# Kernel tuning notes

Hardware: AMD Instinct MI355X
Metric: run time of the kernel (lower is better)

The kernel has to match this reference:

```python
import jax, jax.numpy as jnp
import numpy as np

N, E, D, G, L, ED = 20000, 640000, 128, 128, 5, 7
BN_EPS = 1e-5


def _bn(x, g, b):
    # training-mode BatchNorm1d: biased batch statistics
    m = x.mean(axis=0)
    v = jnp.mean((x - m) ** 2, axis=0)
    return g * (x - m) / jnp.sqrt(v + BN_EPS) + b


def setup_inputs() -> dict:
    key = jax.random.key(0)
    ks = jax.random.split(key, 16)
    s = 0.05
    p = {}
    p["x"] = jax.random.normal(ks[0], (N, D), jnp.float32)
    p["edge_attr"] = jax.random.normal(ks[1], (E, ED), jnp.float32)
    p["edge_index"] = jax.random.randint(ks[2], (2, E), 0, N, jnp.int32)
    p["batch"] = jnp.sort(jax.random.randint(ks[3], (N,), 0, G, jnp.int32))
    p["enc_W"] = jax.random.normal(ks[4], (D, D), jnp.float32) * s
    p["enc_b"] = jnp.zeros((D,), jnp.float32)
    p["vn_emb"] = jnp.zeros((1, D), jnp.float32)  # init.constant_(0)
    p["eps"] = jnp.zeros((L,), jnp.float32)       # GIN eps init 0
    p["edge_W"] = jax.random.normal(ks[5], (L, ED, D), jnp.float32) * s
    p["edge_b"] = jnp.zeros((L, D), jnp.float32)
    p["mlp_W1"] = jax.random.normal(ks[6], (L, D, 2 * D), jnp.float32) * s
    p["mlp_b1"] = jnp.zeros((L, 2 * D), jnp.float32)
    p["mlp_bn1_g"] = jnp.ones((L, 2 * D), jnp.float32)
    p["mlp_bn1_b"] = jnp.zeros((L, 2 * D), jnp.float32)
    p["mlp_W2"] = jax.random.normal(ks[7], (L, 2 * D, D), jnp.float32) * s
    p["mlp_b2"] = jnp.zeros((L, D), jnp.float32)
    p["bn_g"] = jnp.ones((L, D), jnp.float32)
    p["bn_b"] = jnp.zeros((L, D), jnp.float32)
    p["vn_W1"] = jax.random.normal(ks[8], (L - 1, D, 2 * D), jnp.float32) * s
    p["vn_b1"] = jnp.zeros((L - 1, 2 * D), jnp.float32)
    p["vn_bn1_g"] = jnp.ones((L - 1, 2 * D), jnp.float32)
    p["vn_bn1_b"] = jnp.zeros((L - 1, 2 * D), jnp.float32)
    p["vn_W2"] = jax.random.normal(ks[9], (L - 1, 2 * D, D), jnp.float32) * s
    p["vn_b2"] = jnp.zeros((L - 1, D), jnp.float32)
    p["vn_bn2_g"] = jnp.ones((L - 1, D), jnp.float32)
    p["vn_bn2_b"] = jnp.zeros((L - 1, D), jnp.float32)
    return p


def reference(x, edge_attr, edge_index, batch, enc_W, enc_b, vn_emb, eps,
              edge_W, edge_b, mlp_W1, mlp_b1, mlp_bn1_g, mlp_bn1_b, mlp_W2,
              mlp_b2, bn_g, bn_b, vn_W1, vn_b1, vn_bn1_g, vn_bn1_b, vn_W2,
              vn_b2, vn_bn2_g, vn_bn2_b):
    src, dst = edge_index[0], edge_index[1]
    h = x @ enc_W + enc_b                       # node_encoder (Linear)
    vn = jnp.broadcast_to(vn_emb[0], (G, D))    # virtual node per graph, init 0
    for l in range(L):
        h_in = h + vn[batch]                    # gather virtual node into nodes
        # GINConv: message = relu(x_j + edge_emb), aggr='add'
        eemb = edge_attr @ edge_W[l] + edge_b[l]            # [E, D]
        msg = jax.nn.relu(h_in[src] + eemb)                 # [E, D]
        agg = jax.ops.segment_sum(msg, dst, num_segments=N) # scatter-add
        z = (1.0 + eps[l]) * h_in + agg
        z = jax.nn.relu(_bn(z @ mlp_W1[l] + mlp_b1[l], mlp_bn1_g[l], mlp_bn1_b[l]))
        z = z @ mlp_W2[l] + mlp_b2[l]
        hn = _bn(z, bn_g[l], bn_b[l])           # outer BatchNorm1d
        if l < L - 1:
            hn = jax.nn.relu(hn)                # relu on all but last layer
            # virtual node update: global_add_pool over h_list[layer] (= h_in)
            pooled = jax.ops.segment_sum(h_in, batch, num_segments=G) + vn
            t = jax.nn.relu(_bn(pooled @ vn_W1[l] + vn_b1[l], vn_bn1_g[l], vn_bn1_b[l]))
            vn = jax.nn.relu(_bn(t @ vn_W2[l] + vn_b2[l], vn_bn2_g[l], vn_bn2_b[l]))
        h = hn
    return h  # JK='last' node representation [N, D]
```

## Files before the change

### kernel.cpp

```cpp
#include <hip/hip_runtime.h>

#define N_NODES 20000
#define N_EDGES 640000
#define DIM 128
#define NGRAPH 128
#define NLAYER 5
#define EDIM 7
#define TWO_D 256

typedef __bf16 bf16x8 __attribute__((ext_vector_type(8)));
typedef __bf16 bf16x4 __attribute__((ext_vector_type(4)));
typedef __bf16 bf16x2 __attribute__((ext_vector_type(2)));
typedef float  f32x4  __attribute__((ext_vector_type(4)));

__device__ __forceinline__ f32x4 mfma16(bf16x8 a, bf16x8 b, f32x4 c) {
  return __builtin_amdgcn_mfma_f32_16x16x32_bf16(a, b, c, 0, 0, 0);
}

__global__ void k_hist(const int* __restrict__ dst, int* __restrict__ counts) {
  int e = blockIdx.x * blockDim.x + threadIdx.x;
  if (e < N_EDGES) atomicAdd(&counts[dst[e]], 1);
}

__global__ __launch_bounds__(1024) void k_scanA(const int* __restrict__ counts,
    int* __restrict__ local, int* __restrict__ bsum) {
  __shared__ int sd[1024];
  int b = blockIdx.x, tid = threadIdx.x;
  int i = b * 1024 + tid;
  int v = (i < N_NODES) ? counts[i] : 0;
  sd[tid] = v;
  __syncthreads();
  for (int ofs = 1; ofs < 1024; ofs <<= 1) {
    int t = (tid >= ofs) ? sd[tid - ofs] : 0;
    __syncthreads();
    sd[tid] += t;
    __syncthreads();
  }
  if (i <= N_NODES) local[i] = sd[tid] - v;
  if (tid == 1023) bsum[b] = sd[1023];
}

__global__ void k_scanB(int* __restrict__ bsum, int* __restrict__ carry,
                        int* __restrict__ offsets) {
  if (threadIdx.x == 0) {
    int run = 0;
    for (int b = 0; b < 20; ++b) { carry[b] = run; run += bsum[b]; }
    offsets[N_NODES] = run;
  }
}

__global__ __launch_bounds__(1024) void k_scanC(const int* __restrict__ local,
    const int* __restrict__ carry, int* __restrict__ offsets) {
  int i = blockIdx.x * 1024 + threadIdx.x;
  if (i < N_NODES) offsets[i] = local[i] + carry[i >> 10];
}

__global__ void k_fillA(const int* __restrict__ dstArr, const int* __restrict__ offsets,
                        int* __restrict__ cursor, int* __restrict__ perm) {
  int e = blockIdx.x * blockDim.x + threadIdx.x;
  if (e >= N_EDGES) return;
  int d = dstArr[e];
  int p = offsets[d] + atomicAdd(&cursor[d], 1);
  perm[p] = e;
}

__global__ void k_fillB(const int* __restrict__ perm, const int* __restrict__ srcArr,
                        const float* __restrict__ edge_attr,
                        int* __restrict__ csr_src, __bf16* __restrict__ ea_csr) {
  int i = blockIdx.x * blockDim.x + threadIdx.x;
  if (i >= N_EDGES) return;
  int e = perm[i];
  csr_src[i] = srcArr[e];
  const float* ea = edge_attr + (size_t)e * EDIM;
  bf16x8 v;
#pragma unroll
  for (int k = 0; k < EDIM; ++k) v[k] = (__bf16)ea[k];
  v[7] = (__bf16)0.f;
  *(bf16x8*)(ea_csr + (size_t)i * 8) = v;
}

__global__ void k_gs(const int* __restrict__ batch, int* __restrict__ gs) {
  int g = threadIdx.x;
  if (g > NGRAPH) return;
  if (g == NGRAPH) { gs[NGRAPH] = N_NODES; return; }
  int lo = 0, hi = N_NODES;
  while (lo < hi) { int mid = (lo + hi) >> 1; if (batch[mid] < g) lo = mid + 1; else hi = mid; }
  gs[g] = lo;
}

__global__ void k_convT2(const float* __restrict__ src, __bf16* __restrict__ dst_hi,
                         __bf16* __restrict__ dst_lo, int K, int C, int layers) {
  int total = layers * K * C;
  for (int i = blockIdx.x * blockDim.x + threadIdx.x; i < total;
       i += gridDim.x * blockDim.x) {
    int l = i / (K * C);
    int rem = i - l * K * C;
    int k = rem / C;
    int c = rem - k * C;
    float v = src[i];
    __bf16 hi = (__bf16)v;
    __bf16 lo = (__bf16)(v - (float)hi);
    size_t o = (size_t)l * K * C + (size_t)c * K + k;
    dst_hi[o] = hi;
    dst_lo[o] = lo;
  }
}

__global__ void k_vninit(const float* __restrict__ vn_emb, float* __restrict__ vn) {
  int i = blockIdx.x * blockDim.x + threadIdx.x;
  if (i < NGRAPH * DIM) vn[i] = vn_emb[i & (DIM - 1)];
}

__global__ __launch_bounds__(128) void k_enc(const float* __restrict__ x,
    const __bf16* __restrict__ encT_hi, const __bf16* __restrict__ encT_lo,
    const float* __restrict__ enc_b, const float* __restrict__ vn_emb,
    float* __restrict__ h_in, __bf16* __restrict__ h_bf) {
  int lane = threadIdx.x & 63, wid = threadIdx.x >> 6;
  int rbase = blockIdx.x * 32 + wid * 16;
  int r = rbase + (lane & 15);
  int ko = (lane >> 4) * 8;
  const float* xr = x + (size_t)r * DIM;
  bf16x8 a_hi[4], a_lo[4];
#pragma unroll
  for (int ks = 0; ks < 4; ++ks) {
    f32x4 v0 = *(const f32x4*)(xr + ks * 32 + ko);
    f32x4 v1 = *(const f32x4*)(xr + ks * 32 + ko + 4);
    bf16x8 th, tl;
#pragma unroll
    for (int j = 0; j < 4; ++j) {
      th[j] = (__bf16)v0[j];     tl[j] = (__bf16)(v0[j] - (float)th[j]);
      th[4+j] = (__bf16)v1[j];   tl[4+j] = (__bf16)(v1[j] - (float)th[4+j]);
    }
    a_hi[ks] = th; a_lo[ks] = tl;
  }
  const f32x4 fz = {0.f, 0.f, 0.f, 0.f};
  f32x4 acc[8];
#pragma unroll
  for (int nf = 0; nf < 8; ++nf) acc[nf] = fz;
#pragma unroll
  for (int nf = 0; nf < 8; ++nf) {
    size_t wrow = (size_t)(nf * 16 + (lane & 15)) * DIM + ko;
    const __bf16* bh = encT_hi + wrow;
    const __bf16* bl = encT_lo + wrow;
#pragma unroll
    for (int ks = 0; ks < 4; ++ks) {
      bf16x8 wh = *(const bf16x8*)(bh + ks * 32);
      bf16x8 wl = *(const bf16x8*)(bl + ks * 32);
      acc[nf] = mfma16(a_hi[ks], wh, acc[nf]);
      acc[nf] = mfma16(a_lo[ks], wh, acc[nf]);
      acc[nf] = mfma16(a_hi[ks], wl, acc[nf]);
    }
  }
  int c0 = lane & 15;
  int rr = rbase + (lane >> 4) * 4;
#pragma unroll
  for (int nf = 0; nf < 8; ++nf) {
    int c = nf * 16 + c0;
    float bias = enc_b[c] + vn_emb[c];
#pragma unroll
    for (int j = 0; j < 4; ++j) {
      float v = acc[nf][j] + bias;
      h_in[(size_t)(rr + j) * DIM + c] = v;
      h_bf[(size_t)(rr + j) * DIM + c] = (__bf16)v;
    }
  }
}

__global__ __launch_bounds__(1024) void k_pool(const __bf16* __restrict__ h_bf,
    const int* __restrict__ gs, const float* __restrict__ vnbuf,
    const float* __restrict__ vnr, const float* __restrict__ sv2,
    const float* __restrict__ qv2, const float* __restrict__ bn2g,
    const float* __restrict__ bn2b, int use_stats,
    float* __restrict__ pooled) {
  __shared__ float red[8][DIM];
  __shared__ float vns[DIM];
  int tid = threadIdx.x;
  int g = blockIdx.x;
  if (tid < DIM) {
    if (use_stats) {
      float s = 0.f, q = 0.f;
#pragma unroll
      for (int rep = 0; rep < 8; ++rep) { s += sv2[rep * DIM + tid]; q += qv2[rep * DIM + tid]; }
      float m = s * (1.f / NGRAPH);
      float var = q * (1.f / NGRAPH) - m * m;
      float a = bn2g[tid] / sqrtf(var + 1e-5f);
      vns[tid] = fmaxf(vnr[g * DIM + tid] * a + (bn2b[tid] - m * a), 0.f);
    } else {
      vns[tid] = vnbuf[g * DIM + tid];
    }
  }
  __syncthreads();
  int d = tid & 127, slot = tid >> 7;
  int lo = gs[g], hi = gs[g + 1];
  float acc = 0.f;
  for (int n = lo + slot; n < hi; n += 8)
    acc += (float)h_bf[(size_t)n * DIM + d];
  red[slot][d] = acc;
  __syncthreads();
  if (slot == 0) {
    float t = vns[d];
#pragma unroll
    for (int s2 = 0; s2 < 8; ++s2) t += red[s2][d];
    pooled[g * DIM + d] = t;
  }
}

__global__ __launch_bounds__(256) void k_agg(const __bf16* __restrict__ h_bf,
    const float* __restrict__ h_in, const int* __restrict__ offsets,
    const int* __restrict__ csr_src, const __bf16* __restrict__ ea_csr,
    const float* __restrict__ eW, const float* __restrict__ eB,
    const float* __restrict__ eps, int l,
    __bf16* __restrict__ z_hi, __bf16* __restrict__ z_lo) {
  int tid = threadIdx.x;
  int lane = tid & 63, w = tid >> 6;
  int l2 = lane * 2;
  int n = blockIdx.x * 4 + w;
  float w0[EDIM], w1[EDIM];
#pragma unroll
  for (int k = 0; k < EDIM; ++k) {
    float2 wv = *(const float2*)(eW + k * DIM + l2);
    w0[k] = wv.x; w1[k] = wv.y;
  }
  float2 ebv = *(const float2*)(eB + l2);
  int off = offsets[n], end = offsets[n + 1];
  float acc0 = 0.f, acc1 = 0.f;

  auto edge = [&](int iu) {
    int s = csr_src[iu];
    const unsigned* eu = (const unsigned*)(ea_csr + (size_t)iu * 8);
    unsigned u0 = eu[0], u1 = eu[1], u2 = eu[2], u3 = eu[3];
    unsigned hv = *(const unsigned*)(h_bf + (size_t)s * DIM + l2);
    float e0 = __builtin_bit_cast(float, u0 << 16);
    float e1 = __builtin_bit_cast(float, u0 & 0xffff0000u);
    float e2 = __builtin_bit_cast(float, u1 << 16);
    float e3 = __builtin_bit_cast(float, u1 & 0xffff0000u);
    float e4 = __builtin_bit_cast(float, u2 << 16);
    float e5 = __builtin_bit_cast(float, u2 & 0xffff0000u);
    float e6 = __builtin_bit_cast(float, u3 << 16);
    float m0 = __builtin_bit_cast(float, hv << 16) + ebv.x;
    float m1 = __builtin_bit_cast(float, hv & 0xffff0000u) + ebv.y;
    m0 = fmaf(e0, w0[0], m0); m1 = fmaf(e0, w1[0], m1);
    m0 = fmaf(e1, w0[1], m0); m1 = fmaf(e1, w1[1], m1);
    m0 = fmaf(e2, w0[2], m0); m1 = fmaf(e2, w1[2], m1);
    m0 = fmaf(e3, w0[3], m0); m1 = fmaf(e3, w1[3], m1);
    m0 = fmaf(e4, w0[4], m0); m1 = fmaf(e4, w1[4], m1);
    m0 = fmaf(e5, w0[5], m0); m1 = fmaf(e5, w1[5], m1);
    m0 = fmaf(e6, w0[6], m0); m1 = fmaf(e6, w1[6], m1);
    acc0 += fmaxf(m0, 0.f);
    acc1 += fmaxf(m1, 0.f);
  };

  int i = off;
  for (; i + 7 < end; i += 8) {
    int iu = __builtin_amdgcn_readfirstlane(i);
    edge(iu);     edge(iu + 1); edge(iu + 2); edge(iu + 3);
    edge(iu + 4); edge(iu + 5); edge(iu + 6); edge(iu + 7);
  }
  for (; i < end; ++i) {
    edge(__builtin_amdgcn_readfirstlane(i));
  }
  float epsv = 1.f + eps[l];
  float2 hs = *(const float2*)(h_in + (size_t)n * DIM + l2);
  float v0 = epsv * hs.x + acc0;
  float v1 = epsv * hs.y + acc1;
  __bf16 hi0 = (__bf16)v0, hi1 = (__bf16)v1;
  bf16x2 zh; zh[0] = hi0; zh[1] = hi1;
  bf16x2 zl; zl[0] = (__bf16)(v0 - (float)hi0); zl[1] = (__bf16)(v1 - (float)hi1);
  *(bf16x2*)(z_hi + (size_t)n * DIM + l2) = zh;
  *(bf16x2*)(z_lo + (size_t)n * DIM + l2) = zl;
}

__global__ __launch_bounds__(256) void k_gemm1(const __bf16* __restrict__ z_hi,
    const __bf16* __restrict__ z_lo,
    const __bf16* __restrict__ W1T_hi, const __bf16* __restrict__ W1T_lo,
    const float* __restrict__ b1,
    float* __restrict__ y1, float* __restrict__ s1, float* __restrict__ q1) {
  int tid = threadIdx.x;
  int lane = tid & 63, wid = tid >> 6;
  int rowH = wid >> 1, colH = wid & 1;
  int rbase = blockIdx.x * 32 + rowH * 16;
  int r = rbase + (lane & 15);
  int ko = (lane >> 4) * 8;
  bf16x8 a_hi[4], a_lo[4];
#pragma unroll
  for (int ks = 0; ks < 4; ++ks) {
    a_hi[ks] = *(const bf16x8*)(z_hi + (size_t)r * DIM + ks * 32 + ko);
    a_lo[ks] = *(const bf16x8*)(z_lo + (size_t)r * DIM + ks * 32 + ko);
  }
  const f32x4 fz = {0.f, 0.f, 0.f, 0.f};
  f32x4 acc[8];
#pragma unroll
  for (int nf8 = 0; nf8 < 8; ++nf8) acc[nf8] = fz;
#pragma unroll
  for (int nf8 = 0; nf8 < 8; ++nf8) {
    int nf = colH * 8 + nf8;
    size_t wrow = (size_t)(nf * 16 + (lane & 15)) * DIM + ko;
    const __bf16* bh = W1T_hi + wrow;
    const __bf16* bl = W1T_lo + wrow;
#pragma unroll
    for (int ks = 0; ks < 4; ++ks) {
      bf16x8 wh = *(const bf16x8*)(bh + ks * 32);
      bf16x8 wl = *(const bf16x8*)(bl + ks * 32);
      acc[nf8] = mfma16(a_hi[ks], wh, acc[nf8]);
      acc[nf8] = mfma16(a_lo[ks], wh, acc[nf8]);
      acc[nf8] = mfma16(a_hi[ks], wl, acc[nf8]);
    }
  }
  int c0 = lane & 15;
  int rr = rbase + (lane >> 4) * 4;
  int rep = blockIdx.x & 7;
#pragma unroll
  for (int nf8 = 0; nf8 < 8; ++nf8) {
    int c = (colH * 8 + nf8) * 16 + c0;
    float bias = b1[c];
    float s = 0.f, q = 0.f;
#pragma unroll
    for (int j = 0; j < 4; ++j) {
      float v = acc[nf8][j] + bias;
      y1[(size_t)(rr + j) * TWO_D + c] = v;
      s += v; q += v * v;
    }
    s += __shfl_xor(s, 16); s += __shfl_xor(s, 32);
    q += __shfl_xor(q, 16); q += __shfl_xor(q, 32);
    if (lane < 16) {
      atomicAdd(&s1[rep * TWO_D + c], s);
      atomicAdd(&q1[rep * TWO_D + c], q);
    }
  }
}

__global__ __launch_bounds__(256) void k_gemm2(const float* __restrict__ y1,
    const __bf16* __restrict__ W2T_hi, const __bf16* __restrict__ W2T_lo,
    const float* __restrict__ b2,
    const float* __restrict__ s1, const float* __restrict__ q1,
    const float* __restrict__ bn1g, const float* __restrict__ bn1b,
    float* __restrict__ y2, float* __restrict__ s2, float* __restrict__ q2) {
  __shared__ float sc1s[TWO_D], sh1s[TWO_D];
  int tid = threadIdx.x;
  {
    int c = tid;
    float s = 0.f, q = 0.f;
#pragma unroll
    for (int rep = 0; rep < 8; ++rep) { s += s1[rep * TWO_D + c]; q += q1[rep * TWO_D + c]; }
    float m = s * (1.f / N_NODES);
    float var = q * (1.f / N_NODES) - m * m;
    float a = bn1g[c] / sqrtf(var + 1e-5f);
    sc1s[c] = a; sh1s[c] = bn1b[c] - m * a;
  }
  __syncthreads();
  int lane = tid & 63, wid = tid >> 6;
  int rowH = wid >> 1, colH = wid & 1;
  int rbase = blockIdx.x * 32 + rowH * 16;
  int r = rbase + (lane & 15);
  int ko = (lane >> 4) * 8;
  bf16x8 a_hi[8], a_lo[8];
#pragma unroll
  for (int ks = 0; ks < 8; ++ks) {
    int kb = ks * 32 + ko;
    f32x4 r0 = *(const f32x4*)(y1 + (size_t)r * TWO_D + kb);
    f32x4 r1 = *(const f32x4*)(y1 + (size_t)r * TWO_D + kb + 4);
    f32x4 sc0 = *(const f32x4*)(&sc1s[kb]);
    f32x4 sc1 = *(const f32x4*)(&sc1s[kb + 4]);
    f32x4 sh0 = *(const f32x4*)(&sh1s[kb]);
    f32x4 sh1 = *(const f32x4*)(&sh1s[kb + 4]);
    bf16x8 th, tl;
#pragma unroll
    for (int j = 0; j < 4; ++j) {
      float v0 = fmaxf(r0[j] * sc0[j] + sh0[j], 0.f);
      float v1 = fmaxf(r1[j] * sc1[j] + sh1[j], 0.f);
      th[j] = (__bf16)v0;     tl[j] = (__bf16)(v0 - (float)th[j]);
      th[4+j] = (__bf16)v1;   tl[4+j] = (__bf16)(v1 - (float)th[4+j]);
    }
    a_hi[ks] = th; a_lo[ks] = tl;
  }
  const f32x4 fz = {0.f, 0.f, 0.f, 0.f};
  f32x4 acc[4];
#pragma unroll
  for (int nf4 = 0; nf4 < 4; ++nf4) acc[nf4] = fz;
#pragma unroll
  for (int nf4 = 0; nf4 < 4; ++nf4) {
    int nf = colH * 4 + nf4;
    size_t wrow = (size_t)(nf * 16 + (lane & 15)) * TWO_D + ko;
    const __bf16* bh = W2T_hi + wrow;
    const __bf16* bl = W2T_lo + wrow;
#pragma unroll
    for (int ks = 0; ks < 8; ++ks) {
      bf16x8 wh = *(const bf16x8*)(bh + ks * 32);
      bf16x8 wl = *(const bf16x8*)(bl + ks * 32);
      acc[nf4] = mfma16(a_hi[ks], wh, acc[nf4]);
      acc[nf4] = mfma16(a_lo[ks], wh, acc[nf4]);
      acc[nf4] = mfma16(a_hi[ks], wl, acc[nf4]);
    }
  }
  int c0 = lane & 15;
  int rr = rbase + (lane >> 4) * 4;
  int rep = blockIdx.x & 7;
#pragma unroll
  for (int nf4 = 0; nf4 < 4; ++nf4) {
    int c = (colH * 4 + nf4) * 16 + c0;
    float bias = b2[c];
    float s = 0.f, q = 0.f;
#pragma unroll
    for (int j = 0; j < 4; ++j) {
      float v = acc[nf4][j] + bias;
      y2[(size_t)(rr + j) * DIM + c] = v;
      s += v; q += v * v;
    }
    s += __shfl_xor(s, 16); s += __shfl_xor(s, 32);
    q += __shfl_xor(q, 16); q += __shfl_xor(q, 32);
    if (lane < 16) {
      atomicAdd(&s2[rep * DIM + c], s);
      atomicAdd(&q2[rep * DIM + c], q);
    }
  }
}

__global__ __launch_bounds__(256) void k_vgemm1(const float* __restrict__ pooled,
    const float* __restrict__ W1, const float* __restrict__ b1,
    float* __restrict__ tv, float* __restrict__ sv1, float* __restrict__ qv1) {
  __shared__ float row[DIM];
  int g = blockIdx.x, tid = threadIdx.x;
  if (tid < DIM) row[tid] = pooled[g * DIM + tid];
  __syncthreads();
  int c = tid;
  float acc = b1[c];
  for (int k = 0; k < DIM; ++k) acc = fmaf(row[k], W1[k * TWO_D + c], acc);
  tv[g * TWO_D + c] = acc;
  int rep = g & 7;
  atomicAdd(&sv1[rep * TWO_D + c], acc);
  atomicAdd(&qv1[rep * TWO_D + c], acc * acc);
}

__global__ __launch_bounds__(256) void k_vgemm2(const float* __restrict__ tv,
    const float* __restrict__ sv1, const float* __restrict__ qv1,
    const float* __restrict__ bn1g, const float* __restrict__ bn1b,
    const float* __restrict__ W2, const float* __restrict__ b2,
    float* __restrict__ vnr, float* __restrict__ sv2, float* __restrict__ qv2) {
  __shared__ float trow[TWO_D];
  int g = blockIdx.x, tid = threadIdx.x;
  {
    float s = 0.f, q = 0.f;
#pragma unroll
    for (int rep = 0; rep < 8; ++rep) { s += sv1[rep * TWO_D + tid]; q += qv1[rep * TWO_D + tid]; }
    float m = s * (1.f / NGRAPH);
    float var = q * (1.f / NGRAPH) - m * m;
    float a = bn1g[tid] / sqrtf(var + 1e-5f);
    trow[tid] = fmaxf(tv[g * TWO_D + tid] * a + (bn1b[tid] - m * a), 0.f);
  }
  __syncthreads();
  if (tid < DIM) {
    float acc = b2[tid];
    for (int k = 0; k < TWO_D; ++k) acc = fmaf(trow[k], W2[k * DIM + tid], acc);
    vnr[g * DIM + tid] = acc;
    int rep = g & 7;
    atomicAdd(&sv2[rep * DIM + tid], acc);
    atomicAdd(&qv2[rep * DIM + tid], acc * acc);
  }
}

__global__ __launch_bounds__(256) void k_bn2hin(const float* __restrict__ y2,
    const float* __restrict__ s2, const float* __restrict__ q2,
    const float* __restrict__ bng, const float* __restrict__ bnb,
    const float* __restrict__ vnr, const float* __restrict__ sv2,
    const float* __restrict__ qv2, const float* __restrict__ vbn2g,
    const float* __restrict__ vbn2b, const int* __restrict__ batch,
    float* __restrict__ h_in, __bf16* __restrict__ h_bf) {
  __shared__ float sc2s[DIM], sh2s[DIM], scvn[DIM], shvn[DIM];
  int tid = threadIdx.x;
  if (tid < DIM) {
    float s = 0.f, q = 0.f;
#pragma unroll
    for (int rep = 0; rep < 8; ++rep) { s += s2[rep * DIM + tid]; q += q2[rep * DIM + tid]; }
    float m = s * (1.f / N_NODES);
    float var = q * (1.f / N_NODES) - m * m;
    float a = bng[tid] / sqrtf(var + 1e-5f);
    sc2s[tid] = a; sh2s[tid] = bnb[tid] - m * a;
    float sv = 0.f, qv = 0.f;
#pragma unroll
    for (int rep = 0; rep < 8; ++rep) { sv += sv2[rep * DIM + tid]; qv += qv2[rep * DIM + tid]; }
    float mv = sv * (1.f / NGRAPH);
    float varv = qv * (1.f / NGRAPH) - mv * mv;
    float av = vbn2g[tid] / sqrtf(varv + 1e-5f);
    scvn[tid] = av; shvn[tid] = vbn2b[tid] - mv * av;
  }
  __syncthreads();
  int idx = blockIdx.x * 256 + tid;
  if (idx >= N_NODES * (DIM / 4)) return;
  int c4 = idx & 31;
  int row = idx >> 5;
  f32x4 y = ((const f32x4*)y2)[idx];
  f32x4 scv = ((const f32x4*)sc2s)[c4];
  f32x4 shv = ((const f32x4*)sh2s)[c4];
  f32x4 vsc = ((const f32x4*)scvn)[c4];
  f32x4 vsh = ((const f32x4*)shvn)[c4];
  int b = batch[row];
  f32x4 vr = ((const f32x4*)vnr)[b * 32 + c4];
  f32x4 o;
  bf16x4 ob;
#pragma unroll
  for (int j = 0; j < 4; ++j) {
    float vnv = fmaxf(vr[j] * vsc[j] + vsh[j], 0.f);
    o[j] = fmaxf(y[j] * scv[j] + shv[j], 0.f) + vnv;
    ob[j] = (__bf16)o[j];
  }
  ((f32x4*)h_in)[idx] = o;
  ((bf16x4*)h_bf)[idx] = ob;
}

__global__ __launch_bounds__(256) void k_out(const float* __restrict__ y2,
    const float* __restrict__ s2, const float* __restrict__ q2,
    const float* __restrict__ bng, const float* __restrict__ bnb,
    float* __restrict__ out) {
  __shared__ float sc2s[DIM], sh2s[DIM];
  int tid = threadIdx.x;
  if (tid < DIM) {
    float s = 0.f, q = 0.f;
#pragma unroll
    for (int rep = 0; rep < 8; ++rep) { s += s2[rep * DIM + tid]; q += q2[rep * DIM + tid]; }
    float m = s * (1.f / N_NODES);
    float var = q * (1.f / N_NODES) - m * m;
    float a = bng[tid] / sqrtf(var + 1e-5f);
    sc2s[tid] = a; sh2s[tid] = bnb[tid] - m * a;
  }
  __syncthreads();
  int idx = blockIdx.x * 256 + tid;
  if (idx >= N_NODES * (DIM / 4)) return;
  int c4 = idx & 31;
  f32x4 y = ((const f32x4*)y2)[idx];
  f32x4 scv = ((const f32x4*)sc2s)[c4];
  f32x4 shv = ((const f32x4*)sh2s)[c4];
  f32x4 o;
#pragma unroll
  for (int j = 0; j < 4; ++j) o[j] = y[j] * scv[j] + shv[j];
  ((f32x4*)out)[idx] = o;
}

extern "C" void kernel_launch(void* const* d_in, const int* in_sizes, int n_in,
                              void* d_out, int out_size, void* d_ws, size_t ws_size,
                              hipStream_t stream) {
  const float* x         = (const float*)d_in[0];
  const float* edge_attr = (const float*)d_in[1];
  const int*   edge_index= (const int*)d_in[2];
  const int*   batch     = (const int*)d_in[3];
  const float* enc_W     = (const float*)d_in[4];
  const float* enc_b     = (const float*)d_in[5];
  const float* vn_emb    = (const float*)d_in[6];
  const float* eps       = (const float*)d_in[7];
  const float* edge_W    = (const float*)d_in[8];
  const float* edge_b    = (const float*)d_in[9];
  const float* mlp_W1    = (const float*)d_in[10];
  const float* mlp_b1    = (const float*)d_in[11];
  const float* mlp_bn1_g = (const float*)d_in[12];
  const float* mlp_bn1_b = (const float*)d_in[13];
  const float* mlp_W2    = (const float*)d_in[14];
  const float* mlp_b2    = (const float*)d_in[15];
  const float* bn_g      = (const float*)d_in[16];
  const float* bn_b      = (const float*)d_in[17];
  const float* vn_W1     = (const float*)d_in[18];
  const float* vn_b1     = (const float*)d_in[19];
  const float* vn_bn1_g  = (const float*)d_in[20];
  const float* vn_bn1_b  = (const float*)d_in[21];
  const float* vn_W2     = (const float*)d_in[22];
  const float* vn_b2     = (const float*)d_in[23];
  const float* vn_bn2_g  = (const float*)d_in[24];
  const float* vn_bn2_b  = (const float*)d_in[25];

  char* wsb = (char*)d_ws;
  size_t off = 0;
  auto take = [&](size_t bytes) -> void* {
    void* p = wsb + off;
    off += (bytes + 255) & ~(size_t)255;
    return p;
  };
  float*  h_in    = (float*)take((size_t)N_NODES * DIM * 4);
  float*  y2      = (float*)take((size_t)N_NODES * DIM * 4);
  float*  y1      = (float*)take((size_t)N_NODES * TWO_D * 4);
  __bf16* h_bf    = (__bf16*)y1;
  __bf16* z_hi    = (__bf16*)take((size_t)N_NODES * DIM * 2);
  __bf16* z_lo    = (__bf16*)take((size_t)N_NODES * DIM * 2);
  int*    csr_src = (int*)take((size_t)N_EDGES * 4);
  __bf16* ea_csr  = (__bf16*)take((size_t)N_EDGES * 8 * 2);
  int*    perm    = (int*)take((size_t)N_EDGES * 4);
  int*    counts  = (int*)take((size_t)2 * N_NODES * 4);
  int*    cursor  = counts + N_NODES;
  int*    offsets = (int*)take((size_t)(N_NODES + 1) * 4);
  int*    slocal  = (int*)take((size_t)(N_NODES + 1024) * 4);
  int*    sbsum   = (int*)take(64 * 4);
  int*    scarry  = sbsum + 32;
  int*    gs      = (int*)take((size_t)(NGRAPH + 1) * 4);
  float*  pooled  = (float*)take((size_t)NGRAPH * DIM * 4);
  float*  tv      = (float*)take((size_t)NGRAPH * TWO_D * 4);
  float*  vnr     = (float*)take((size_t)NGRAPH * DIM * 4);
  float*  vn0     = (float*)take((size_t)NGRAPH * DIM * 4);
  float*  stats   = (float*)take((size_t)NLAYER * 12288 * 4);
  __bf16* encT_hi = (__bf16*)take((size_t)DIM * DIM * 2);
  __bf16* encT_lo = (__bf16*)take((size_t)DIM * DIM * 2);
  __bf16* W1T_hi  = (__bf16*)take((size_t)NLAYER * DIM * TWO_D * 2);
  __bf16* W1T_lo  = (__bf16*)take((size_t)NLAYER * DIM * TWO_D * 2);
  __bf16* W2T_hi  = (__bf16*)take((size_t)NLAYER * TWO_D * DIM * 2);
  __bf16* W2T_lo  = (__bf16*)take((size_t)NLAYER * TWO_D * DIM * 2);
  if (off > ws_size) return;

  const int* srcArr = edge_index;
  const int* dstArr = edge_index + N_EDGES;

  hipMemsetAsync(counts, 0, (size_t)2 * N_NODES * 4, stream);
  hipMemsetAsync(stats, 0, (size_t)NLAYER * 12288 * 4, stream);

  k_hist<<<N_EDGES / 256, 256, 0, stream>>>(dstArr, counts);
  k_scanA<<<20, 1024, 0, stream>>>(counts, slocal, sbsum);
  k_scanB<<<1, 64, 0, stream>>>(sbsum, scarry, offsets);
  k_scanC<<<20, 1024, 0, stream>>>(slocal, scarry, offsets);
  k_fillA<<<N_EDGES / 256, 256, 0, stream>>>(dstArr, offsets, cursor, perm);
  k_fillB<<<N_EDGES / 256, 256, 0, stream>>>(perm, srcArr, edge_attr, csr_src, ea_csr);
  k_gs<<<1, 256, 0, stream>>>(batch, gs);
  k_convT2<<<128, 256, 0, stream>>>(enc_W, encT_hi, encT_lo, DIM, DIM, 1);
  k_convT2<<<128, 256, 0, stream>>>(mlp_W1, W1T_hi, W1T_lo, DIM, TWO_D, NLAYER);
  k_convT2<<<128, 256, 0, stream>>>(mlp_W2, W2T_hi, W2T_lo, TWO_D, DIM, NLAYER);
  k_vninit<<<(NGRAPH * DIM) / 256, 256, 0, stream>>>(vn_emb, vn0);
  k_enc<<<N_NODES / 32, 128, 0, stream>>>(x, encT_hi, encT_lo, enc_b, vn_emb, h_in, h_bf);

  for (int l = 0; l < NLAYER; ++l) {
    float* s1  = stats + (size_t)l * 12288;
    float* q1  = s1 + 2048;
    float* s2  = s1 + 4096;
    float* q2  = s1 + 5120;
    float* sv1 = s1 + 6144;
    float* qv1 = s1 + 8192;
    float* sv2 = s1 + 10240;
    float* qv2 = s1 + 11264;
    if (l < NLAYER - 1) {
      if (l == 0)
        k_pool<<<NGRAPH, 1024, 0, stream>>>(h_bf, gs, vn0, vn0, nullptr, nullptr,
            nullptr, nullptr, 0, pooled);
      else {
        float* psv2 = stats + (size_t)(l - 1) * 12288 + 10240;
        float* pqv2 = stats + (size_t)(l - 1) * 12288 + 11264;
        k_pool<<<NGRAPH, 1024, 0, stream>>>(h_bf, gs, vn0, vnr, psv2, pqv2,
            vn_bn2_g + (size_t)(l - 1) * DIM, vn_bn2_b + (size_t)(l - 1) * DIM, 1, pooled);
      }
    }
    k_agg<<<N_NODES / 4, 256, 0, stream>>>(h_bf, h_in, offsets, csr_src, ea_csr,
        edge_W + (size_t)l * EDIM * DIM, edge_b + (size_t)l * DIM, eps, l, z_hi, z_lo);
    k_gemm1<<<N_NODES / 32, 256, 0, stream>>>(z_hi, z_lo,
        W1T_hi + (size_t)l * DIM * TWO_D, W1T_lo + (size_t)l * DIM * TWO_D,
        mlp_b1 + (size_t)l * TWO_D, y1, s1, q1);
    k_gemm2<<<N_NODES / 32, 256, 0, stream>>>(y1,
        W2T_hi + (size_t)l * TWO_D * DIM, W2T_lo + (size_t)l * TWO_D * DIM,
        mlp_b2 + (size_t)l * DIM, s1, q1,
        mlp_bn1_g + (size_t)l * TWO_D, mlp_bn1_b + (size_t)l * TWO_D,
        y2, s2, q2);
    if (l < NLAYER - 1) {
      k_vgemm1<<<NGRAPH, 256, 0, stream>>>(pooled, vn_W1 + (size_t)l * DIM * TWO_D,
          vn_b1 + (size_t)l * TWO_D, tv, sv1, qv1);
      k_vgemm2<<<NGRAPH, 256, 0, stream>>>(tv, sv1, qv1,
          vn_bn1_g + (size_t)l * TWO_D, vn_bn1_b + (size_t)l * TWO_D,
          vn_W2 + (size_t)l * TWO_D * DIM, vn_b2 + (size_t)l * DIM,
          vnr, sv2, qv2);
      k_bn2hin<<<(N_NODES * 32) / 256, 256, 0, stream>>>(y2, s2, q2,
          bn_g + (size_t)l * DIM, bn_b + (size_t)l * DIM,
          vnr, sv2, qv2, vn_bn2_g + (size_t)l * DIM, vn_bn2_b + (size_t)l * DIM,
          batch, h_in, h_bf);
    } else {
      k_out<<<(N_NODES * 32) / 256, 256, 0, stream>>>(y2, s2, q2,
          bn_g + (size_t)l * DIM, bn_b + (size_t)l * DIM, (float*)d_out);
    }
  }
}
```

Before: 738.9 us.

## Store activations as bf16 hi/lo pairs and merge setup kernels

Result: no change. 740.5 us (+0.2%).

```diff
diff --git a/kernel.cpp b/kernel.cpp
--- a/kernel.cpp
+++ b/kernel.cpp
@@ -41,11 +41,21 @@
 }
 
 __global__ void k_scanB(int* __restrict__ bsum, int* __restrict__ carry,
-                        int* __restrict__ offsets) {
-  if (threadIdx.x == 0) {
+                        int* __restrict__ offsets, const int* __restrict__ batch,
+                        int* __restrict__ gs) {
+  int tid = threadIdx.x;
+  if (tid == 0) {
     int run = 0;
     for (int b = 0; b < 20; ++b) { carry[b] = run; run += bsum[b]; }
     offsets[N_NODES] = run;
+  }
+  if (tid <= NGRAPH) {
+    if (tid == NGRAPH) gs[NGRAPH] = N_NODES;
+    else {
+      int lo = 0, hi = N_NODES;
+      while (lo < hi) { int mid = (lo + hi) >> 1; if (batch[mid] < tid) lo = mid + 1; else hi = mid; }
+      gs[tid] = lo;
+    }
   }
 }
 
@@ -79,30 +89,30 @@
   *(bf16x8*)(ea_csr + (size_t)i * 8) = v;
 }
 
-__global__ void k_gs(const int* __restrict__ batch, int* __restrict__ gs) {
-  int g = threadIdx.x;
-  if (g > NGRAPH) return;
-  if (g == NGRAPH) { gs[NGRAPH] = N_NODES; return; }
-  int lo = 0, hi = N_NODES;
-  while (lo < hi) { int mid = (lo + hi) >> 1; if (batch[mid] < g) lo = mid + 1; else hi = mid; }
-  gs[g] = lo;
-}
-
-__global__ void k_convT2(const float* __restrict__ src, __bf16* __restrict__ dst_hi,
-                         __bf16* __restrict__ dst_lo, int K, int C, int layers) {
-  int total = layers * K * C;
+__global__ void k_convAll(const float* __restrict__ encW, const float* __restrict__ W1,
+    const float* __restrict__ W2,
+    __bf16* __restrict__ encT_hi, __bf16* __restrict__ encT_lo,
+    __bf16* __restrict__ W1T_hi, __bf16* __restrict__ W1T_lo,
+    __bf16* __restrict__ W2T_hi, __bf16* __restrict__ W2T_lo) {
+  const int t1 = DIM * DIM;
+  const int t2 = NLAYER * DIM * TWO_D;
+  const int total = t1 + t2 + t2;
   for (int i = blockIdx.x * blockDim.x + threadIdx.x; i < total;
        i += gridDim.x * blockDim.x) {
-    int l = i / (K * C);
-    int rem = i - l * K * C;
+    const float* src; __bf16 *dh, *dl; int K, C, idx;
+    if (i < t1)            { src = encW; dh = encT_hi; dl = encT_lo; K = DIM;   C = DIM;   idx = i; }
+    else if (i < t1 + t2)  { src = W1;   dh = W1T_hi;  dl = W1T_lo;  K = DIM;   C = TWO_D; idx = i - t1; }
+    else                   { src = W2;   dh = W2T_hi;  dl = W2T_lo;  K = TWO_D; C = DIM;   idx = i - t1 - t2; }
+    int l = idx / (K * C);
+    int rem = idx - l * K * C;
     int k = rem / C;
     int c = rem - k * C;
-    float v = src[i];
+    float v = src[idx];
     __bf16 hi = (__bf16)v;
     __bf16 lo = (__bf16)(v - (float)hi);
     size_t o = (size_t)l * K * C + (size_t)c * K + k;
-    dst_hi[o] = hi;
-    dst_lo[o] = lo;
+    dh[o] = hi;
+    dl[o] = lo;
   }
 }
 
@@ -114,7 +124,7 @@
 __global__ __launch_bounds__(128) void k_enc(const float* __restrict__ x,
     const __bf16* __restrict__ encT_hi, const __bf16* __restrict__ encT_lo,
     const float* __restrict__ enc_b, const float* __restrict__ vn_emb,
-    float* __restrict__ h_in, __bf16* __restrict__ h_bf) {
+    __bf16* __restrict__ h_hi, __bf16* __restrict__ h_lo) {
   int lane = threadIdx.x & 63, wid = threadIdx.x >> 6;
   int rbase = blockIdx.x * 32 + wid * 16;
   int r = rbase + (lane & 15);
@@ -160,13 +170,14 @@
 #pragma unroll
     for (int j = 0; j < 4; ++j) {
       float v = acc[nf][j] + bias;
-      h_in[(size_t)(rr + j) * DIM + c] = v;
-      h_bf[(size_t)(rr + j) * DIM + c] = (__bf16)v;
-    }
-  }
-}
-
-__global__ __launch_bounds__(1024) void k_pool(const __bf16* __restrict__ h_bf,
+      __bf16 hi = (__bf16)v;
+      h_hi[(size_t)(rr + j) * DIM + c] = hi;
+      h_lo[(size_t)(rr + j) * DIM + c] = (__bf16)(v - (float)hi);
+    }
+  }
+}
+
+__global__ __launch_bounds__(1024) void k_pool(const __bf16* __restrict__ h_hi,
     const int* __restrict__ gs, const float* __restrict__ vnbuf,
     const float* __restrict__ vnr, const float* __restrict__ sv2,
     const float* __restrict__ qv2, const float* __restrict__ bn2g,
@@ -194,7 +205,7 @@
   int lo = gs[g], hi = gs[g + 1];
   float acc = 0.f;
   for (int n = lo + slot; n < hi; n += 8)
-    acc += (float)h_bf[(size_t)n * DIM + d];
+    acc += (float)h_hi[(size_t)n * DIM + d];
   red[slot][d] = acc;
   __syncthreads();
   if (slot == 0) {
@@ -205,8 +216,8 @@
   }
 }
 
-__global__ __launch_bounds__(256) void k_agg(const __bf16* __restrict__ h_bf,
-    const float* __restrict__ h_in, const int* __restrict__ offsets,
+__global__ __launch_bounds__(256) void k_agg(const __bf16* __restrict__ h_hi,
+    const __bf16* __restrict__ h_lo, const int* __restrict__ offsets,
     const int* __restrict__ csr_src, const __bf16* __restrict__ ea_csr,
     const float* __restrict__ eW, const float* __restrict__ eB,
     const float* __restrict__ eps, int l,
@@ -229,7 +240,7 @@
     int s = csr_src[iu];
     const unsigned* eu = (const unsigned*)(ea_csr + (size_t)iu * 8);
     unsigned u0 = eu[0], u1 = eu[1], u2 = eu[2], u3 = eu[3];
-    unsigned hv = *(const unsigned*)(h_bf + (size_t)s * DIM + l2);
+    unsigned hv = *(const unsigned*)(h_hi + (size_t)s * DIM + l2);
     float e0 = __builtin_bit_cast(float, u0 << 16);
     float e1 = __builtin_bit_cast(float, u0 & 0xffff0000u);
     float e2 = __builtin_bit_cast(float, u1 << 16);
@@ -251,18 +262,23 @@
   };
 
   int i = off;
-  for (; i + 7 < end; i += 8) {
+  for (; i + 3 < end; i += 4) {
     int iu = __builtin_amdgcn_readfirstlane(i);
-    edge(iu);     edge(iu + 1); edge(iu + 2); edge(iu + 3);
-    edge(iu + 4); edge(iu + 5); edge(iu + 6); edge(iu + 7);
+    edge(iu);
+    edge(iu + 1);
+    edge(iu + 2);
+    edge(iu + 3);
   }
   for (; i < end; ++i) {
     edge(__builtin_amdgcn_readfirstlane(i));
   }
   float epsv = 1.f + eps[l];
-  float2 hs = *(const float2*)(h_in + (size_t)n * DIM + l2);
-  float v0 = epsv * hs.x + acc0;
-  float v1 = epsv * hs.y + acc1;
+  unsigned hvh = *(const unsigned*)(h_hi + (size_t)n * DIM + l2);
+  unsigned hvl = *(const unsigned*)(h_lo + (size_t)n * DIM + l2);
+  float s0 = __builtin_bit_cast(float, hvh << 16) + __builtin_bit_cast(float, hvl << 16);
+  float s1 = __builtin_bit_cast(float, hvh & 0xffff0000u) + __builtin_bit_cast(float, hvl & 0xffff0000u);
+  float v0 = epsv * s0 + acc0;
+  float v1 = epsv * s1 + acc1;
   __bf16 hi0 = (__bf16)v0, hi1 = (__bf16)v1;
   bf16x2 zh; zh[0] = hi0; zh[1] = hi1;
   bf16x2 zl; zl[0] = (__bf16)(v0 - (float)hi0); zl[1] = (__bf16)(v1 - (float)hi1);
@@ -274,7 +290,8 @@
     const __bf16* __restrict__ z_lo,
     const __bf16* __restrict__ W1T_hi, const __bf16* __restrict__ W1T_lo,
     const float* __restrict__ b1,
-    float* __restrict__ y1, float* __restrict__ s1, float* __restrict__ q1) {
+    __bf16* __restrict__ y1h, __bf16* __restrict__ y1l,
+    float* __restrict__ s1, float* __restrict__ q1) {
   int tid = threadIdx.x;
   int lane = tid & 63, wid = tid >> 6;
   int rowH = wid >> 1, colH = wid & 1;
@@ -317,7 +334,9 @@
 #pragma unroll
     for (int j = 0; j < 4; ++j) {
       float v = acc[nf8][j] + bias;
-      y1[(size_t)(rr + j) * TWO_D + c] = v;
+      __bf16 hi = (__bf16)v;
+      y1h[(size_t)(rr + j) * TWO_D + c] = hi;
+      y1l[(size_t)(rr + j) * TWO_D + c] = (__bf16)(v - (float)hi);
       s += v; q += v * v;
     }
     s += __shfl_xor(s, 16); s += __shfl_xor(s, 32);
@@ -329,7 +348,8 @@
   }
 }
 
-__global__ __launch_bounds__(256) void k_gemm2(const float* __restrict__ y1,
+__global__ __launch_bounds__(256) void k_gemm2(const __bf16* __restrict__ y1h,
+    const __bf16* __restrict__ y1l,
     const __bf16* __restrict__ W2T_hi, const __bf16* __restrict__ W2T_lo,
     const float* __restrict__ b2,
     const float* __restrict__ s1, const float* __restrict__ q1,
@@ -357,8 +377,8 @@
 #pragma unroll
   for (int ks = 0; ks < 8; ++ks) {
     int kb = ks * 32 + ko;
-    f32x4 r0 = *(const f32x4*)(y1 + (size_t)r * TWO_D + kb);
-    f32x4 r1 = *(const f32x4*)(y1 + (size_t)r * TWO_D + kb + 4);
+    bf16x8 rh = *(const bf16x8*)(y1h + (size_t)r * TWO_D + kb);
+    bf16x8 rl = *(const bf16x8*)(y1l + (size_t)r * TWO_D + kb);
     f32x4 sc0 = *(const f32x4*)(&sc1s[kb]);
     f32x4 sc1 = *(const f32x4*)(&sc1s[kb + 4]);
     f32x4 sh0 = *(const f32x4*)(&sh1s[kb]);
@@ -366,8 +386,10 @@
     bf16x8 th, tl;
 #pragma unroll
     for (int j = 0; j < 4; ++j) {
-      float v0 = fmaxf(r0[j] * sc0[j] + sh0[j], 0.f);
-      float v1 = fmaxf(r1[j] * sc1[j] + sh1[j], 0.f);
+      float r0 = (float)rh[j] + (float)rl[j];
+      float r1 = (float)rh[4 + j] + (float)rl[4 + j];
+      float v0 = fmaxf(r0 * sc0[j] + sh0[j], 0.f);
+      float v1 = fmaxf(r1 * sc1[j] + sh1[j], 0.f);
       th[j] = (__bf16)v0;     tl[j] = (__bf16)(v0 - (float)th[j]);
       th[4+j] = (__bf16)v1;   tl[4+j] = (__bf16)(v1 - (float)th[4+j]);
     }
@@ -464,7 +486,7 @@
     const float* __restrict__ vnr, const float* __restrict__ sv2,
     const float* __restrict__ qv2, const float* __restrict__ vbn2g,
     const float* __restrict__ vbn2b, const int* __restrict__ batch,
-    float* __restrict__ h_in, __bf16* __restrict__ h_bf) {
+    __bf16* __restrict__ h_hi, __bf16* __restrict__ h_lo) {
   __shared__ float sc2s[DIM], sh2s[DIM], scvn[DIM], shvn[DIM];
   int tid = threadIdx.x;
   if (tid < DIM) {
@@ -495,16 +517,17 @@
   f32x4 vsh = ((const f32x4*)shvn)[c4];
   int b = batch[row];
   f32x4 vr = ((const f32x4*)vnr)[b * 32 + c4];
-  f32x4 o;
-  bf16x4 ob;
+  bf16x4 oh, ol;
 #pragma unroll
   for (int j = 0; j < 4; ++j) {
     float vnv = fmaxf(vr[j] * vsc[j] + vsh[j], 0.f);
-    o[j] = fmaxf(y[j] * scv[j] + shv[j], 0.f) + vnv;
-    ob[j] = (__bf16)o[j];
-  }
-  ((f32x4*)h_in)[idx] = o;
-  ((bf16x4*)h_bf)[idx] = ob;
+    float o = fmaxf(y[j] * scv[j] + shv[j], 0.f) + vnv;
+    __bf16 hi = (__bf16)o;
+    oh[j] = hi;
+    ol[j] = (__bf16)(o - (float)hi);
+  }
+  ((bf16x4*)h_hi)[idx] = oh;
+  ((bf16x4*)h_lo)[idx] = ol;
 }
 
 __global__ __launch_bounds__(256) void k_out(const float* __restrict__ y2,
@@ -572,17 +595,19 @@
     off += (bytes + 255) & ~(size_t)255;
     return p;
   };
-  float*  h_in    = (float*)take((size_t)N_NODES * DIM * 4);
+  int*    counts  = (int*)take((size_t)2 * N_NODES * 4);
+  int*    cursor  = counts + N_NODES;
+  float*  stats   = (float*)take((size_t)NLAYER * 12288 * 4);
+  __bf16* h_hi    = (__bf16*)take((size_t)N_NODES * DIM * 2);
+  __bf16* h_lo    = (__bf16*)take((size_t)N_NODES * DIM * 2);
   float*  y2      = (float*)take((size_t)N_NODES * DIM * 4);
-  float*  y1      = (float*)take((size_t)N_NODES * TWO_D * 4);
-  __bf16* h_bf    = (__bf16*)y1;
+  __bf16* y1h     = (__bf16*)take((size_t)N_NODES * TWO_D * 2);
+  __bf16* y1l     = (__bf16*)take((size_t)N_NODES * TWO_D * 2);
   __bf16* z_hi    = (__bf16*)take((size_t)N_NODES * DIM * 2);
   __bf16* z_lo    = (__bf16*)take((size_t)N_NODES * DIM * 2);
   int*    csr_src = (int*)take((size_t)N_EDGES * 4);
   __bf16* ea_csr  = (__bf16*)take((size_t)N_EDGES * 8 * 2);
   int*    perm    = (int*)take((size_t)N_EDGES * 4);
-  int*    counts  = (int*)take((size_t)2 * N_NODES * 4);
-  int*    cursor  = counts + N_NODES;
   int*    offsets = (int*)take((size_t)(N_NODES + 1) * 4);
   int*    slocal  = (int*)take((size_t)(N_NODES + 1024) * 4);
   int*    sbsum   = (int*)take(64 * 4);
@@ -592,7 +617,6 @@
   float*  tv      = (float*)take((size_t)NGRAPH * TWO_D * 4);
   float*  vnr     = (float*)take((size_t)NGRAPH * DIM * 4);
   float*  vn0     = (float*)take((size_t)NGRAPH * DIM * 4);
-  float*  stats   = (float*)take((size_t)NLAYER * 12288 * 4);
   __bf16* encT_hi = (__bf16*)take((size_t)DIM * DIM * 2);
   __bf16* encT_lo = (__bf16*)take((size_t)DIM * DIM * 2);
   __bf16* W1T_hi  = (__bf16*)take((size_t)NLAYER * DIM * TWO_D * 2);
@@ -604,21 +628,18 @@
   const int* srcArr = edge_index;
   const int* dstArr = edge_index + N_EDGES;
 
-  hipMemsetAsync(counts, 0, (size_t)2 * N_NODES * 4, stream);
-  hipMemsetAsync(stats, 0, (size_t)NLAYER * 12288 * 4, stream);
+  hipMemsetAsync(counts, 0, (size_t)2 * N_NODES * 4 + (size_t)NLAYER * 12288 * 4, stream);
 
   k_hist<<<N_EDGES / 256, 256, 0, stream>>>(dstArr, counts);
   k_scanA<<<20, 1024, 0, stream>>>(counts, slocal, sbsum);
-  k_scanB<<<1, 64, 0, stream>>>(sbsum, scarry, offsets);
+  k_scanB<<<1, 256, 0, stream>>>(sbsum, scarry, offsets, batch, gs);
   k_scanC<<<20, 1024, 0, stream>>>(slocal, scarry, offsets);
   k_fillA<<<N_EDGES / 256, 256, 0, stream>>>(dstArr, offsets, cursor, perm);
   k_fillB<<<N_EDGES / 256, 256, 0, stream>>>(perm, srcArr, edge_attr, csr_src, ea_csr);
-  k_gs<<<1, 256, 0, stream>>>(batch, gs);
-  k_convT2<<<128, 256, 0, stream>>>(enc_W, encT_hi, encT_lo, DIM, DIM, 1);
-  k_convT2<<<128, 256, 0, stream>>>(mlp_W1, W1T_hi, W1T_lo, DIM, TWO_D, NLAYER);
-  k_convT2<<<128, 256, 0, stream>>>(mlp_W2, W2T_hi, W2T_lo, TWO_D, DIM, NLAYER);
+  k_convAll<<<336, 1024, 0, stream>>>(enc_W, mlp_W1, mlp_W2,
+      encT_hi, encT_lo, W1T_hi, W1T_lo, W2T_hi, W2T_lo);
   k_vninit<<<(NGRAPH * DIM) / 256, 256, 0, stream>>>(vn_emb, vn0);
-  k_enc<<<N_NODES / 32, 128, 0, stream>>>(x, encT_hi, encT_lo, enc_b, vn_emb, h_in, h_bf);
+  k_enc<<<N_NODES / 32, 128, 0, stream>>>(x, encT_hi, encT_lo, enc_b, vn_emb, h_hi, h_lo);
 
   for (int l = 0; l < NLAYER; ++l) {
     float* s1  = stats + (size_t)l * 12288;
@@ -631,21 +652,21 @@
     float* qv2 = s1 + 11264;
     if (l < NLAYER - 1) {
       if (l == 0)
-        k_pool<<<NGRAPH, 1024, 0, stream>>>(h_bf, gs, vn0, vn0, nullptr, nullptr,
+        k_pool<<<NGRAPH, 1024, 0, stream>>>(h_hi, gs, vn0, vn0, nullptr, nullptr,
             nullptr, nullptr, 0, pooled);
       else {
         float* psv2 = stats + (size_t)(l - 1) * 12288 + 10240;
         float* pqv2 = stats + (size_t)(l - 1) * 12288 + 11264;
-        k_pool<<<NGRAPH, 1024, 0, stream>>>(h_bf, gs, vn0, vnr, psv2, pqv2,
+        k_pool<<<NGRAPH, 1024, 0, stream>>>(h_hi, gs, vn0, vnr, psv2, pqv2,
             vn_bn2_g + (size_t)(l - 1) * DIM, vn_bn2_b + (size_t)(l - 1) * DIM, 1, pooled);
       }
     }
-    k_agg<<<N_NODES / 4, 256, 0, stream>>>(h_bf, h_in, offsets, csr_src, ea_csr,
+    k_agg<<<N_NODES / 4, 256, 0, stream>>>(h_hi, h_lo, offsets, csr_src, ea_csr,
         edge_W + (size_t)l * EDIM * DIM, edge_b + (size_t)l * DIM, eps, l, z_hi, z_lo);
     k_gemm1<<<N_NODES / 32, 256, 0, stream>>>(z_hi, z_lo,
         W1T_hi + (size_t)l * DIM * TWO_D, W1T_lo + (size_t)l * DIM * TWO_D,
-        mlp_b1 + (size_t)l * TWO_D, y1, s1, q1);
-    k_gemm2<<<N_NODES / 32, 256, 0, stream>>>(y1,
+        mlp_b1 + (size_t)l * TWO_D, y1h, y1l, s1, q1);
+    k_gemm2<<<N_NODES / 32, 256, 0, stream>>>(y1h, y1l,
         W2T_hi + (size_t)l * TWO_D * DIM, W2T_lo + (size_t)l * TWO_D * DIM,
         mlp_b2 + (size_t)l * DIM, s1, q1,
         mlp_bn1_g + (size_t)l * TWO_D, mlp_bn1_b + (size_t)l * TWO_D,
@@ -660,7 +681,7 @@
       k_bn2hin<<<(N_NODES * 32) / 256, 256, 0, stream>>>(y2, s2, q2,
           bn_g + (size_t)l * DIM, bn_b + (size_t)l * DIM,
           vnr, sv2, qv2, vn_bn2_g + (size_t)l * DIM, vn_bn2_b + (size_t)l * DIM,
-          batch, h_in, h_bf);
+          batch, h_hi, h_lo);
     } else {
       k_out<<<(N_NODES * 32) / 256, 256, 0, stream>>>(y2, s2, q2,
           bn_g + (size_t)l * DIM, bn_b + (size_t)l * DIM, (float*)d_out);
```
